# Kernel tuning notes

Measured on AMD Instinct MI355X. Metric: run time of the kernel, lower is better.

The kernel has to match this reference:

```python
import jax, jax.numpy as jnp
import numpy as np

HEAD_NUM = 16
D_MODEL = 1024
D_K = D_MODEL // HEAD_NUM


def setup_inputs() -> dict:
    key = jax.random.key(0)
    ks = jax.random.split(key, 11)
    B, S = 4, 2048
    def xavier(k, shape):
        fan_in, fan_out = shape[1], shape[0]
        lim = np.sqrt(6.0 / (fan_in + fan_out))
        return jax.random.uniform(k, shape, jnp.float32, -lim, lim)
    return {
        "query": jax.random.normal(ks[0], (B, S, D_MODEL), jnp.float32),
        "key": jax.random.normal(ks[1], (B, S, D_MODEL), jnp.float32),
        "value": jax.random.normal(ks[2], (B, S, D_MODEL), jnp.float32),
        "w_q": xavier(ks[3], (D_MODEL, D_MODEL)),
        "b_q": jnp.zeros((D_MODEL,), jnp.float32),
        "w_k": xavier(ks[4], (D_MODEL, D_MODEL)),
        "b_k": jnp.zeros((D_MODEL,), jnp.float32),
        "w_v": xavier(ks[5], (D_MODEL, D_MODEL)),
        "b_v": jnp.zeros((D_MODEL,), jnp.float32),
        "w_o": xavier(ks[6], (D_MODEL, D_MODEL)),
        "b_o": jnp.zeros((D_MODEL,), jnp.float32),
    }


def reference(query, key, value, w_q, b_q, w_k, b_k, w_v, b_v, w_o, b_o):
    B = query.shape[0]
    # Linear projections (torch Linear: x @ W^T + b), split into heads: [B,H,S,Dk]
    def proj(x, w, b):
        y = x @ w.T + b
        return y.reshape(B, -1, HEAD_NUM, D_K).transpose(0, 2, 1, 3)
    q = proj(query, w_q, b_q)
    k = proj(key, w_k, b_k)
    v = proj(value, w_v, b_v)
    # scaled dot-product attention with full score matrix [B,H,Sq,Sk]
    scores = jnp.einsum('bhqd,bhkd->bhqk', q, k) / jnp.sqrt(jnp.float32(D_K))
    attn = jax.nn.softmax(scores, axis=-1)
    out = jnp.einsum('bhqk,bhkd->bhqd', attn, v)
    out = out.transpose(0, 2, 1, 3).reshape(B, -1, HEAD_NUM * D_K)
    return out @ w_o.T + b_o
```

## Files before the change

kernel.cpp:

```cpp
#include <hip/hip_runtime.h>
#include <hip/hip_bf16.h>
#include <stdint.h>

#define HN 16
#define DMODEL 1024
#define DKH 64
#define SEQ 2048

typedef __attribute__((ext_vector_type(8))) short short8v;
typedef __attribute__((ext_vector_type(4))) short short4v;
typedef __attribute__((ext_vector_type(4))) float f32x4;

__device__ __forceinline__ short bfc(float x) {
    __hip_bfloat16 h = __float2bfloat16(x);
    return *reinterpret_cast<short*>(&h);
}

__device__ __forceinline__ void gll16(const void* g, void* l) {
    __builtin_amdgcn_global_load_lds(
        (const __attribute__((address_space(1))) unsigned int*)g,
        (__attribute__((address_space(3))) unsigned int*)l, 16, 0, 0);
}

__global__ void cvtw_kernel(const float* __restrict__ w0, const float* __restrict__ w1,
                            const float* __restrict__ w2, const float* __restrict__ w3,
                            short* __restrict__ dst, float scale0) {
    const int z = blockIdx.z;
    const float* src = z == 0 ? w0 : z == 1 ? w1 : z == 2 ? w2 : w3;
    short* d = dst + ((size_t)z << 20);
    const float scale = (z == 0) ? scale0 : 1.f;
    const int i = blockIdx.x * blockDim.x + threadIdx.x;
    const float4 v0 = ((const float4*)src)[i * 2];
    const float4 v1 = ((const float4*)src)[i * 2 + 1];
    short8v o;
    o[0] = bfc(v0.x * scale); o[1] = bfc(v0.y * scale);
    o[2] = bfc(v0.z * scale); o[3] = bfc(v0.w * scale);
    o[4] = bfc(v1.x * scale); o[5] = bfc(v1.y * scale);
    o[6] = bfc(v1.z * scale); o[7] = bfc(v1.w * scale);
    ((short8v*)d)[i] = o;
}

__global__ void cvtx_kernel(const float* __restrict__ x0, const float* __restrict__ x1,
                            const float* __restrict__ x2, short* __restrict__ dst,
                            unsigned zstride) {
    const int z = blockIdx.z;
    const float* src = z == 0 ? x0 : z == 1 ? x1 : x2;
    short* d = dst + (size_t)z * zstride;
    const int i = blockIdx.x * blockDim.x + threadIdx.x;
    const float4 v0 = ((const float4*)src)[i * 2];
    const float4 v1 = ((const float4*)src)[i * 2 + 1];
    short8v o;
    o[0] = bfc(v0.x); o[1] = bfc(v0.y); o[2] = bfc(v0.z); o[3] = bfc(v0.w);
    o[4] = bfc(v1.x); o[5] = bfc(v1.y); o[6] = bfc(v1.z); o[7] = bfc(v1.w);
    ((short8v*)d)[i] = o;
}

__global__ __launch_bounds__(256) void gemm_proj(
    const short* __restrict__ Ax, unsigned zstride, int z0,
    const short* __restrict__ wb,
    const float* __restrict__ bq, const float* __restrict__ bk, const float* __restrict__ bv,
    short* __restrict__ qb, short* __restrict__ kb, short* __restrict__ vtb, float c1)
{
    constexpr int K = DMODEL;
    const int z = z0 + blockIdx.z;
    const short* A    = Ax + (size_t)blockIdx.z * zstride;
    const short* W    = wb + ((size_t)z << 20);
    const float* bias = z == 0 ? bq : z == 1 ? bk : bv;
    const float bscale = (z == 0) ? c1 : 1.f;

    __shared__ __align__(16) short As[2][8192];
    __shared__ __align__(16) short Bs[2][8192];
    const int t = threadIdx.x, lane = t & 63;
    const int w = t >> 6, wr = w >> 1, wc = w & 1;
    const int m0 = blockIdx.y * 128, n0 = blockIdx.x * 128;
    const int r16 = lane & 15, g = lane >> 4;

    f32x4 acc[4][4];
    #pragma unroll
    for (int i = 0; i < 4; ++i)
        #pragma unroll
        for (int j = 0; j < 4; ++j) { acc[i][j][0]=0.f; acc[i][j][1]=0.f; acc[i][j][2]=0.f; acc[i][j][3]=0.f; }

    const int sr = t >> 3, sx = ((t & 7) ^ (sr & 7)) * 8;
    const short* Asrc = A + (size_t)(m0 + sr) * K + sx;
    const short* Bsrc = W + (size_t)(n0 + sr) * K + sx;

    #pragma unroll
    for (int q4 = 0; q4 < 4; ++q4) {
        gll16(Asrc + (size_t)(q4*32) * K, &As[0][0] + t*8 + q4*2048);
        gll16(Bsrc + (size_t)(q4*32) * K, &Bs[0][0] + t*8 + q4*2048);
    }
    __syncthreads();

    int cur = 0;
    for (int kt = 0; kt < K; kt += 64) {
        if (kt + 64 < K) {
            const int nxt = cur ^ 1;
            #pragma unroll
            for (int q4 = 0; q4 < 4; ++q4) {
                gll16(Asrc + kt + 64 + (size_t)(q4*32) * K, &As[nxt][0] + t*8 + q4*2048);
                gll16(Bsrc + kt + 64 + (size_t)(q4*32) * K, &Bs[nxt][0] + t*8 + q4*2048);
            }
        }
        const short* Ac = As[cur];
        const short* Bc = Bs[cur];
        #pragma unroll
        for (int kk = 0; kk < 2; ++kk) {
            short8v a[4], b[4];
            #pragma unroll
            for (int i = 0; i < 4; ++i)
                a[i] = *(const short8v*)&Ac[(wr*64 + i*16 + r16)*64 + (((kk*4 + g) ^ (r16 & 7)) * 8)];
            #pragma unroll
            for (int j = 0; j < 4; ++j)
                b[j] = *(const short8v*)&Bc[(wc*64 + j*16 + r16)*64 + (((kk*4 + g) ^ (r16 & 7)) * 8)];
            #pragma unroll
            for (int i = 0; i < 4; ++i)
                #pragma unroll
                for (int j = 0; j < 4; ++j)
                    acc[i][j] = __builtin_amdgcn_mfma_f32_16x16x32_bf16(a[i], b[j], acc[i][j], 0, 0, 0);
        }
        __syncthreads();
        cur ^= 1;
    }

    #pragma unroll
    for (int i = 0; i < 4; ++i) {
        const int mbase = m0 + wr*64 + i*16 + g*4;
        #pragma unroll
        for (int j = 0; j < 4; ++j) {
            const int n = n0 + wc*64 + j*16 + r16;
            const float bvv = bias[n] * bscale;
            const int h = n >> 6, d = n & 63;
            if (z < 2) {
                short* ob = (z == 0) ? qb : kb;
                #pragma unroll
                for (int r = 0; r < 4; ++r) {
                    const int m = mbase + r;
                    const int bb = m >> 11, s = m & 2047;
                    ob[(((size_t)(bb*HN + h)*SEQ + s) << 6) + d] = bfc(acc[i][j][r] + bvv);
                }
            } else {
                const int bb = mbase >> 11, s = mbase & 2047;
                const int blk = s & ~31, b4 = (s >> 2) & 7;
                const int sp = blk | ((((b4 & 3) << 1) | (b4 >> 2)) << 2);
                short4v pk;
                #pragma unroll
                for (int r = 0; r < 4; ++r) pk[r] = bfc(acc[i][j][r] + bvv);
                *(short4v*)&vtb[((size_t)(bb*HN + h)*DKH + d)*SEQ + sp] = pk;
            }
        }
    }
}

__global__ __launch_bounds__(256, 4) void attn_kernel(
    const short* __restrict__ Qb, const short* __restrict__ Kb,
    const short* __restrict__ Vt, short* __restrict__ Ob)
{
    __shared__ __align__(16) short Ks[2][4096];
    __shared__ __align__(16) short Vs[2][4096];
    const int t = threadIdx.x, lane = t & 63, w = t >> 6;
    const int r16 = lane & 15, g = lane >> 4;

    const int bid = blockIdx.x + (blockIdx.y << 4);
    const int wg  = (bid & 7) * 128 + (bid >> 3);
    const int qx  = wg & 15, bh = wg >> 4;

    const size_t hq = (size_t)bh * SEQ * DKH;
    const size_t hv = (size_t)bh * DKH * SEQ;
    const int q0 = qx * 128 + w * 32;

    short8v aq[2][2];
    #pragma unroll
    for (int qm = 0; qm < 2; ++qm)
        #pragma unroll
        for (int h2 = 0; h2 < 2; ++h2)
            aq[qm][h2] = *(const short8v*)(Qb + hq + (size_t)(q0 + qm*16 + r16)*DKH + h2*32 + g*8);

    short8v ones;
    #pragma unroll
    for (int j = 0; j < 8; ++j) ones[j] = (short)0x3F80;

    f32x4 o[2][4], ps[2];
    #pragma unroll
    for (int qm = 0; qm < 2; ++qm) {
        ps[qm][0]=0.f; ps[qm][1]=0.f; ps[qm][2]=0.f; ps[qm][3]=0.f;
        #pragma unroll
        for (int d = 0; d < 4; ++d) { o[qm][d][0]=0.f; o[qm][d][1]=0.f; o[qm][d][2]=0.f; o[qm][d][3]=0.f; }
    }
    const f32x4 zinit = {-4.f, -4.f, -4.f, -4.f};

    const int sr = t >> 3, sx = ((t & 7) ^ (sr & 7)) * 8;
    const short* Ksrc = Kb + hq + (size_t)sr * DKH + sx;
    const short* Vsrc = Vt + hv + (size_t)sr * SEQ + sx;
    const int l0 = t * 8, l1 = 2048 + t * 8;

    gll16(Ksrc,                    &Ks[0][l0]);
    gll16(Ksrc + (size_t)32*DKH,   &Ks[0][l1]);
    gll16(Vsrc,                    &Vs[0][l0]);
    gll16(Vsrc + (size_t)32*SEQ,   &Vs[0][l1]);
    __syncthreads();

    int cur = 0;
    for (int kv0 = 0; kv0 < SEQ; kv0 += 64) {
        if (kv0 + 64 < SEQ) {
            const int nxt = cur ^ 1;
            const int kn = kv0 + 64;
            gll16(Ksrc + (size_t)kn*DKH,        &Ks[nxt][l0]);
            gll16(Ksrc + (size_t)(kn+32)*DKH,   &Ks[nxt][l1]);
            gll16(Vsrc + kn,                    &Vs[nxt][l0]);
            gll16(Vsrc + (size_t)32*SEQ + kn,   &Vs[nxt][l1]);
        }
        const short* Kc = Ks[cur];
        const short* Vc = Vs[cur];

        short8v pa[2][2];
        #pragma unroll
        for (int s2 = 0; s2 < 4; ++s2) {
            const int krow = (s2*16 + r16) * 64;
            short8v ak0 = *(const short8v*)&Kc[krow + ((g       ^ (r16 & 7)) * 8)];
            short8v ak1 = *(const short8v*)&Kc[krow + (((4 + g) ^ (r16 & 7)) * 8)];
            #pragma unroll
            for (int qm = 0; qm < 2; ++qm) {
                f32x4 zz = __builtin_amdgcn_mfma_f32_16x16x32_bf16(ak0, aq[qm][0], zinit, 0, 0, 0);
                zz = __builtin_amdgcn_mfma_f32_16x16x32_bf16(ak1, aq[qm][1], zz, 0, 0, 0);
                pa[qm][s2 >> 1][(s2 & 1)*4 + 0] = bfc(__builtin_amdgcn_exp2f(zz[0]));
                pa[qm][s2 >> 1][(s2 & 1)*4 + 1] = bfc(__builtin_amdgcn_exp2f(zz[1]));
                pa[qm][s2 >> 1][(s2 & 1)*4 + 2] = bfc(__builtin_amdgcn_exp2f(zz[2]));
                pa[qm][s2 >> 1][(s2 & 1)*4 + 3] = bfc(__builtin_amdgcn_exp2f(zz[3]));
            }
        }
        #pragma unroll
        for (int kvh = 0; kvh < 2; ++kvh) {
            #pragma unroll
            for (int qm = 0; qm < 2; ++qm)
                ps[qm] = __builtin_amdgcn_mfma_f32_16x16x32_bf16(pa[qm][kvh], ones, ps[qm], 0, 0, 0);
            #pragma unroll
            for (int dblk = 0; dblk < 4; ++dblk) {
                short8v bvv = *(const short8v*)&Vc[(dblk*16 + r16)*64 + (((kvh*4 + g) ^ (r16 & 7)) * 8)];
                #pragma unroll
                for (int qm = 0; qm < 2; ++qm)
                    o[qm][dblk] = __builtin_amdgcn_mfma_f32_16x16x32_bf16(pa[qm][kvh], bvv, o[qm][dblk], 0, 0, 0);
            }
        }
        __syncthreads();
        cur ^= 1;
    }

    const int bb = bh >> 4, h = bh & 15;
    #pragma unroll
    for (int qm = 0; qm < 2; ++qm)
        #pragma unroll
        for (int r = 0; r < 4; ++r) {
            const float rp = 1.f / ps[qm][r];
            const int q = q0 + qm*16 + g*4 + r;
            #pragma unroll
            for (int dblk = 0; dblk < 4; ++dblk)
                Ob[(size_t)(bb*SEQ + q)*DMODEL + h*DKH + dblk*16 + r16] = bfc(o[qm][dblk][r] * rp);
        }
}

__global__ __launch_bounds__(256) void gemm_out(
    const short* __restrict__ Ain, const short* __restrict__ W,
    const float* __restrict__ bias, float* __restrict__ Out)
{
    constexpr int K = DMODEL;
    __shared__ __align__(16) short As[2][8192];
    __shared__ __align__(16) short Bs[2][8192];
    const int t = threadIdx.x, lane = t & 63;
    const int w = t >> 6, wr = w >> 1, wc = w & 1;
    const int m0 = blockIdx.y * 128, n0 = blockIdx.x * 128;
    const int r16 = lane & 15, g = lane >> 4;

    f32x4 acc[4][4];
    #pragma unroll
    for (int i = 0; i < 4; ++i)
        #pragma unroll
        for (int j = 0; j < 4; ++j) { acc[i][j][0]=0.f; acc[i][j][1]=0.f; acc[i][j][2]=0.f; acc[i][j][3]=0.f; }

    const int sr = t >> 3, sx = ((t & 7) ^ (sr & 7)) * 8;
    const short* Asrc = Ain + (size_t)(m0 + sr) * K + sx;
    const short* Bsrc = W   + (size_t)(n0 + sr) * K + sx;

    #pragma unroll
    for (int q4 = 0; q4 < 4; ++q4) {
        gll16(Asrc + (size_t)(q4*32) * K, &As[0][0] + t*8 + q4*2048);
        gll16(Bsrc + (size_t)(q4*32) * K, &Bs[0][0] + t*8 + q4*2048);
    }
    __syncthreads();

    int cur = 0;
    for (int kt = 0; kt < K; kt += 64) {
        if (kt + 64 < K) {
            const int nxt = cur ^ 1;
            #pragma unroll
            for (int q4 = 0; q4 < 4; ++q4) {
                gll16(Asrc + kt + 64 + (size_t)(q4*32) * K, &As[nxt][0] + t*8 + q4*2048);
                gll16(Bsrc + kt + 64 + (size_t)(q4*32) * K, &Bs[nxt][0] + t*8 + q4*2048);
            }
        }
        const short* Ac = As[cur];
        const short* Bc = Bs[cur];
        #pragma unroll
        for (int kk = 0; kk < 2; ++kk) {
            short8v a[4], b[4];
            #pragma unroll
            for (int i = 0; i < 4; ++i)
                a[i] = *(const short8v*)&Ac[(wr*64 + i*16 + r16)*64 + (((kk*4 + g) ^ (r16 & 7)) * 8)];
            #pragma unroll
            for (int j = 0; j < 4; ++j)
                b[j] = *(const short8v*)&Bc[(wc*64 + j*16 + r16)*64 + (((kk*4 + g) ^ (r16 & 7)) * 8)];
            #pragma unroll
            for (int i = 0; i < 4; ++i)
                #pragma unroll
                for (int j = 0; j < 4; ++j)
                    acc[i][j] = __builtin_amdgcn_mfma_f32_16x16x32_bf16(a[i], b[j], acc[i][j], 0, 0, 0);
        }
        __syncthreads();
        cur ^= 1;
    }

    #pragma unroll
    for (int i = 0; i < 4; ++i) {
        const int mbase = m0 + wr*64 + i*16 + g*4;
        #pragma unroll
        for (int j = 0; j < 4; ++j) {
            const int n = n0 + wc*64 + j*16 + r16;
            const float bvv = bias[n];
            #pragma unroll
            for (int r = 0; r < 4; ++r)
                Out[(size_t)(mbase + r)*DMODEL + n] = acc[i][j][r] + bvv;
        }
    }
}

extern "C" void kernel_launch(void* const* d_in, const int* in_sizes, int n_in,
                              void* d_out, int out_size, void* d_ws, size_t ws_size,
                              hipStream_t stream) {
    const float* query = (const float*)d_in[0];
    const float* key   = (const float*)d_in[1];
    const float* value = (const float*)d_in[2];
    const float* w_q = (const float*)d_in[3];
    const float* b_q = (const float*)d_in[4];
    const float* w_k = (const float*)d_in[5];
    const float* b_k = (const float*)d_in[6];
    const float* w_v = (const float*)d_in[7];
    const float* b_v = (const float*)d_in[8];
    const float* w_o = (const float*)d_in[9];
    const float* b_o = (const float*)d_in[10];

    const float C1 = 0.18033688011112043f;

    short* ws = (short*)d_ws;
    short* wb = ws;
    short* xo = ws + (4u << 20);

    const bool fused = ws_size >= (size_t)104 * 1024 * 1024;
    short *xq, *qb, *kb, *vtb;
    if (fused) {
        xq  = ws + (4u  << 20);
        qb  = ws + (28u << 20);
        kb  = ws + (36u << 20);
        vtb = ws + (44u << 20);
    } else {
        xq  = ws + (4u  << 20);
        qb  = ws + (12u << 20);
        kb  = ws + (20u << 20);
        vtb = ws + (28u << 20);
    }

    cvtw_kernel<<<dim3(512, 1, 4), 256, 0, stream>>>(w_q, w_k, w_v, w_o, wb, C1);

    if (fused) {
        cvtx_kernel<<<dim3(4096, 1, 3), 256, 0, stream>>>(query, key, value, xq, 1u << 23);
        gemm_proj<<<dim3(8, 64, 3), 256, 0, stream>>>(xq, 1u << 23, 0, wb,
                                                      b_q, b_k, b_v, qb, kb, vtb, C1);
    } else {
        const float* xs[3] = {query, key, value};
        for (int z = 0; z < 3; ++z) {
            cvtx_kernel<<<dim3(4096, 1, 1), 256, 0, stream>>>(xs[z], xs[z], xs[z], xq, 0);
            gemm_proj<<<dim3(8, 64, 1), 256, 0, stream>>>(xq, 0, z, wb,
                                                          b_q, b_k, b_v, qb, kb, vtb, C1);
        }
    }

    attn_kernel<<<dim3(16, 64), 256, 0, stream>>>(qb, kb, vtb, xo);

    gemm_out<<<dim3(8, 64), 256, 0, stream>>>(xo, wb + (3u << 20), b_o, (float*)d_out);
}
```

Baseline: 332.7 us.

## Fuse activation fp32-to-bf16 conversion into projection GEMM and swizzle blocks per XCD

```diff
diff --git a/kernel.cpp b/kernel.cpp
--- a/kernel.cpp
+++ b/kernel.cpp
@@ -40,30 +40,21 @@
     ((short8v*)d)[i] = o;
 }
 
-__global__ void cvtx_kernel(const float* __restrict__ x0, const float* __restrict__ x1,
-                            const float* __restrict__ x2, short* __restrict__ dst,
-                            unsigned zstride) {
-    const int z = blockIdx.z;
-    const float* src = z == 0 ? x0 : z == 1 ? x1 : x2;
-    short* d = dst + (size_t)z * zstride;
-    const int i = blockIdx.x * blockDim.x + threadIdx.x;
-    const float4 v0 = ((const float4*)src)[i * 2];
-    const float4 v1 = ((const float4*)src)[i * 2 + 1];
-    short8v o;
-    o[0] = bfc(v0.x); o[1] = bfc(v0.y); o[2] = bfc(v0.z); o[3] = bfc(v0.w);
-    o[4] = bfc(v1.x); o[5] = bfc(v1.y); o[6] = bfc(v1.z); o[7] = bfc(v1.w);
-    ((short8v*)d)[i] = o;
-}
-
 __global__ __launch_bounds__(256) void gemm_proj(
-    const short* __restrict__ Ax, unsigned zstride, int z0,
+    const float* __restrict__ xq, const float* __restrict__ xk, const float* __restrict__ xv,
     const short* __restrict__ wb,
     const float* __restrict__ bq, const float* __restrict__ bk, const float* __restrict__ bv,
     short* __restrict__ qb, short* __restrict__ kb, short* __restrict__ vtb, float c1)
 {
     constexpr int K = DMODEL;
-    const int z = z0 + blockIdx.z;
-    const short* A    = Ax + (size_t)blockIdx.z * zstride;
+    const int id = blockIdx.x;
+    const int cx = id & 7, jj = id >> 3;
+    const int P = cx * 24 + (jj >> 3);
+    const int nblk = jj & 7;
+    const int z = P >> 6, mp = P & 63;
+    const int m0 = mp * 128, n0 = nblk * 128;
+
+    const float* A    = z == 0 ? xq : z == 1 ? xk : xv;
     const short* W    = wb + ((size_t)z << 20);
     const float* bias = z == 0 ? bq : z == 1 ? bk : bv;
     const float bscale = (z == 0) ? c1 : 1.f;
@@ -72,7 +63,6 @@
     __shared__ __align__(16) short Bs[2][8192];
     const int t = threadIdx.x, lane = t & 63;
     const int w = t >> 6, wr = w >> 1, wc = w & 1;
-    const int m0 = blockIdx.y * 128, n0 = blockIdx.x * 128;
     const int r16 = lane & 15, g = lane >> 4;
 
     f32x4 acc[4][4];
@@ -81,26 +71,45 @@
         #pragma unroll
         for (int j = 0; j < 4; ++j) { acc[i][j][0]=0.f; acc[i][j][1]=0.f; acc[i][j][2]=0.f; acc[i][j][3]=0.f; }
 
+    const int ar = t >> 3, ac = t & 7;
+    const int axor = ((ac ^ (ar & 7)) * 8);
+    const float* Asrc = A + (size_t)(m0 + ar) * K + ac * 8;
+    const int aoff = ar * 64 + axor;
     const int sr = t >> 3, sx = ((t & 7) ^ (sr & 7)) * 8;
-    const short* Asrc = A + (size_t)(m0 + sr) * K + sx;
     const short* Bsrc = W + (size_t)(n0 + sr) * K + sx;
 
-    #pragma unroll
-    for (int q4 = 0; q4 < 4; ++q4) {
-        gll16(Asrc + (size_t)(q4*32) * K, &As[0][0] + t*8 + q4*2048);
-        gll16(Bsrc + (size_t)(q4*32) * K, &Bs[0][0] + t*8 + q4*2048);
+    {
+        #pragma unroll
+        for (int q4 = 0; q4 < 4; ++q4)
+            gll16(Bsrc + (size_t)(q4*32) * K, &Bs[0][0] + t*8 + q4*2048);
+        #pragma unroll
+        for (int p = 0; p < 4; ++p) {
+            const float* s = Asrc + (size_t)(p*32) * K;
+            float4 f0 = *(const float4*)s;
+            float4 f1 = *(const float4*)(s + 4);
+            short8v sv;
+            sv[0]=bfc(f0.x); sv[1]=bfc(f0.y); sv[2]=bfc(f0.z); sv[3]=bfc(f0.w);
+            sv[4]=bfc(f1.x); sv[5]=bfc(f1.y); sv[6]=bfc(f1.z); sv[7]=bfc(f1.w);
+            *(short8v*)&As[0][aoff + p*2048] = sv;
+        }
     }
     __syncthreads();
 
     int cur = 0;
     for (int kt = 0; kt < K; kt += 64) {
-        if (kt + 64 < K) {
-            const int nxt = cur ^ 1;
-            #pragma unroll
-            for (int q4 = 0; q4 < 4; ++q4) {
-                gll16(Asrc + kt + 64 + (size_t)(q4*32) * K, &As[nxt][0] + t*8 + q4*2048);
+        const int nxt = cur ^ 1;
+        const bool more = (kt + 64) < K;
+        float4 fa[4][2];
+        if (more) {
+            #pragma unroll
+            for (int p = 0; p < 4; ++p) {
+                const float* s = Asrc + kt + 64 + (size_t)(p*32) * K;
+                fa[p][0] = *(const float4*)s;
+                fa[p][1] = *(const float4*)(s + 4);
+            }
+            #pragma unroll
+            for (int q4 = 0; q4 < 4; ++q4)
                 gll16(Bsrc + kt + 64 + (size_t)(q4*32) * K, &Bs[nxt][0] + t*8 + q4*2048);
-            }
         }
         const short* Ac = As[cur];
         const short* Bc = Bs[cur];
@@ -118,6 +127,15 @@
                 #pragma unroll
                 for (int j = 0; j < 4; ++j)
                     acc[i][j] = __builtin_amdgcn_mfma_f32_16x16x32_bf16(a[i], b[j], acc[i][j], 0, 0, 0);
+        }
+        if (more) {
+            #pragma unroll
+            for (int p = 0; p < 4; ++p) {
+                short8v sv;
+                sv[0]=bfc(fa[p][0].x); sv[1]=bfc(fa[p][0].y); sv[2]=bfc(fa[p][0].z); sv[3]=bfc(fa[p][0].w);
+                sv[4]=bfc(fa[p][1].x); sv[5]=bfc(fa[p][1].y); sv[6]=bfc(fa[p][1].z); sv[7]=bfc(fa[p][1].w);
+                *(short8v*)&As[nxt][aoff + p*2048] = sv;
+            }
         }
         __syncthreads();
         cur ^= 1;
@@ -264,11 +282,15 @@
     const float* __restrict__ bias, float* __restrict__ Out)
 {
     constexpr int K = DMODEL;
+    const int id = blockIdx.x;
+    const int cx = id & 7, jj = id >> 3;
+    const int mp = cx * 8 + (jj >> 3), nblk = jj & 7;
+    const int m0 = mp * 128, n0 = nblk * 128;
+
     __shared__ __align__(16) short As[2][8192];
     __shared__ __align__(16) short Bs[2][8192];
     const int t = threadIdx.x, lane = t & 63;
     const int w = t >> 6, wr = w >> 1, wc = w & 1;
-    const int m0 = blockIdx.y * 128, n0 = blockIdx.x * 128;
     const int r16 = lane & 15, g = lane >> 4;
 
     f32x4 acc[4][4];
@@ -350,40 +372,19 @@
 
     const float C1 = 0.18033688011112043f;
 
-    short* ws = (short*)d_ws;
-    short* wb = ws;
-    short* xo = ws + (4u << 20);
-
-    const bool fused = ws_size >= (size_t)104 * 1024 * 1024;
-    short *xq, *qb, *kb, *vtb;
-    if (fused) {
-        xq  = ws + (4u  << 20);
-        qb  = ws + (28u << 20);
-        kb  = ws + (36u << 20);
-        vtb = ws + (44u << 20);
-    } else {
-        xq  = ws + (4u  << 20);
-        qb  = ws + (12u << 20);
-        kb  = ws + (20u << 20);
-        vtb = ws + (28u << 20);
-    }
+    short* ws  = (short*)d_ws;
+    short* wb  = ws;
+    short* xo  = ws + (4u  << 20);
+    short* qb  = ws + (12u << 20);
+    short* kb  = ws + (20u << 20);
+    short* vtb = ws + (28u << 20);
 
     cvtw_kernel<<<dim3(512, 1, 4), 256, 0, stream>>>(w_q, w_k, w_v, w_o, wb, C1);
 
-    if (fused) {
-        cvtx_kernel<<<dim3(4096, 1, 3), 256, 0, stream>>>(query, key, value, xq, 1u << 23);
-        gemm_proj<<<dim3(8, 64, 3), 256, 0, stream>>>(xq, 1u << 23, 0, wb,
-                                                      b_q, b_k, b_v, qb, kb, vtb, C1);
-    } else {
-        const float* xs[3] = {query, key, value};
-        for (int z = 0; z < 3; ++z) {
-            cvtx_kernel<<<dim3(4096, 1, 1), 256, 0, stream>>>(xs[z], xs[z], xs[z], xq, 0);
-            gemm_proj<<<dim3(8, 64, 1), 256, 0, stream>>>(xq, 0, z, wb,
-                                                          b_q, b_k, b_v, qb, kb, vtb, C1);
-        }
-    }
+    gemm_proj<<<1536, 256, 0, stream>>>(query, key, value, wb,
+                                        b_q, b_k, b_v, qb, kb, vtb, C1);
 
     attn_kernel<<<dim3(16, 64), 256, 0, stream>>>(qb, kb, vtb, xo);
 
-    gemm_out<<<dim3(8, 64), 256, 0, stream>>>(xo, wb + (3u << 20), b_o, (float*)d_out);
-}
+    gemm_out<<<512, 256, 0, stream>>>(xo, wb + (3u << 20), b_o, (float*)d_out);
+}
```

Measured after the change: 347.3 us. +4.4%, slower.
